# Kernel tuning notes

Hardware: AMD Instinct MI355X
Metric: run time of the kernel (lower is better)

Reference implementation:

```python
import jax, jax.numpy as jnp
import numpy as np
from jax import lax

NUM_ROUTING = 3
EPS_SQUASH = 1e-12
EPS_COS = 1e-8


def _squash(x, axis=2):
    norm = jnp.linalg.norm(x, axis=axis, keepdims=True)
    norm_sq = norm * norm
    return x / (norm + EPS_SQUASH) * (norm_sq / (1.0 + norm_sq))


def setup_inputs() -> dict:
    key = jax.random.key(0)
    k1, k2, k3 = jax.random.split(key, 3)
    B, in_dim, in_atoms, D, H, W = 2, 8, 16, 32, 32, 32
    out_dim, out_atoms, ksz = 8, 16, 3
    x = jax.random.normal(k1, (B, in_dim, in_atoms, D, H, W), dtype=jnp.float32)
    conv_w = jax.random.normal(k2, (out_dim * out_atoms, in_atoms, ksz, ksz, ksz), dtype=jnp.float32) * 0.1
    conv_b = jax.random.normal(k3, (out_dim * out_atoms,), dtype=jnp.float32) * 0.01
    biases = jnp.full((out_dim, out_atoms, 1, 1, 1), 0.1, dtype=jnp.float32)
    return {"input_tensor": x, "conv_w": conv_w, "conv_b": conv_b, "biases": biases}


def reference(input_tensor, conv_w, conv_b, biases):
    B, in_dim, in_atoms, D, H, W = input_tensor.shape
    out_dim, out_atoms = biases.shape[0], biases.shape[1]
    # DepthwiseConv4d (share_weight=True): fold (B, in_dim) into batch
    xr = input_tensor.reshape(B * in_dim, in_atoms, D, H, W)
    conv = lax.conv_general_dilated(
        xr, conv_w, window_strides=(1, 1, 1), padding=[(1, 1)] * 3,
        dimension_numbers=("NCDHW", "OIDHW", "NCDHW"))
    conv = conv + conv_b[None, :, None, None, None]
    oD, oH, oW = conv.shape[-3:]
    votes = conv.reshape(B, in_dim, out_dim, out_atoms, oD, oH, oW)
    # dynamic routing
    logits = jnp.zeros((B, in_dim, out_dim, 1, oD, oH, oW), dtype=votes.dtype)
    activation = None
    for i in range(NUM_ROUTING):
        route = jax.nn.softmax(logits, axis=2)
        # sum over input capsules (axis=1) -> [B, out_dim, out_atoms, D, H, W]
        preactivate = jnp.sum(votes * route, axis=1) + biases[None]
        if i + 1 < NUM_ROUTING:
            # cosine similarity along atoms (axis=3)
            p = preactivate[:, None]  # [B,1,out_dim,atoms,D,H,W]
            dot = jnp.sum(p * votes, axis=3)
            pn = jnp.linalg.norm(p, axis=3)
            vn = jnp.linalg.norm(votes, axis=3)
            distances = dot / jnp.maximum(pn * vn, EPS_COS)
            logits = logits + distances[:, :, :, None]
        else:
            activation = _squash(preactivate, axis=2)
    return activation
```

## Files before the change

kernel.cpp:

```cpp
#include <hip/hip_runtime.h>
#include <math.h>


typedef _Float16 half8 __attribute__((ext_vector_type(8)));
typedef _Float16 half4 __attribute__((ext_vector_type(4)));
typedef float f32x4 __attribute__((ext_vector_type(4)));
typedef float f32x2 __attribute__((ext_vector_type(2)));

__device__ __forceinline__ void gload_lds16(const void* g, void* l) {
    __builtin_amdgcn_global_load_lds(
        (const __attribute__((address_space(1))) void*)g,
        (__attribute__((address_space(3))) void*)l, 16, 0, 0);
}

__device__ __forceinline__ float swap1(float x) {
    return __builtin_bit_cast(float, __builtin_amdgcn_update_dpp(
        0, __builtin_bit_cast(int, x), 0xB1, 0xF, 0xF, true));
}
__device__ __forceinline__ f32x2 swap2(f32x2 v) {
    f32x2 r; r[0] = swap1(v[0]); r[1] = swap1(v[1]); return r;
}

__global__ __launch_bounds__(256) void prep_all(const float* __restrict__ x,
                                                const float* __restrict__ cw,
                                                _Float16* __restrict__ xt,
                                                _Float16* __restrict__ wh2) {
    __shared__ _Float16 lds[272 * 136];
    const int t   = threadIdx.x;
    const int bid = blockIdx.x;

    if (bid < 256) {
        const int b  = bid >> 7;
        const int z  = (bid >> 2) & 31;
        const int y0 = (bid & 3) << 3;
        {
            const int rw = t >> 4, u = t & 15;
            const int y = rw >> 1, wp = (rw & 1) * 33;
            *(half8*)&lds[(y * 34 + wp) * 136 + u * 8] = (half8)(_Float16)0.f;
        }
        const float* xb = x + (size_t)b * 4194304 + z * 1024 + y0 * 32;
        #pragma unroll 4
        for (int i = 0; i < 32; i++) {
            const int idx4 = i * 256 + t;
            const int ch = idx4 >> 6;
            const int y  = (idx4 >> 3) & 7;
            const int w4 = idx4 & 7;
            const f32x4 v = *(const f32x4*)(xb + (size_t)ch * 32768 + y * 32 + w4 * 4);
            const int rbase = y * 34 + w4 * 4 + 1;
            #pragma unroll
            for (int e = 0; e < 4; e++)
                lds[(rbase + e) * 136 + ch] = (_Float16)v[e];
        }
        __syncthreads();
        _Float16* dst = xt + ((size_t)((b * 34 + z + 1) * 34 + y0 + 1)) * 34 * 128;
        #pragma unroll
        for (int k = 0; k < 17; k++) {
            const int idx = k * 256 + t;
            const int vox = idx >> 4, u = idx & 15;
            *(half8*)(dst + (size_t)vox * 128 + u * 8) =
                *(const half8*)&lds[vox * 136 + u * 8];
        }
        return;
    }
    if (bid < 520) {
        const int rid = bid - 256;
        const int b = rid / 132, rr = rid - b * 132;
        int zp, yp;
        if (rr < 68) { zp = (rr >= 34) ? 33 : 0; yp = rr % 34; }
        else { const int r2 = rr - 68; zp = 1 + (r2 >> 1); yp = (r2 & 1) ? 33 : 0; }
        _Float16* dst = xt + ((size_t)((b * 34 + zp) * 34 + yp)) * 34 * 128;
        const half8 z8 = (half8)(_Float16)0.f;
        for (int idx = t; idx < 544; idx += 256)
            *(half8*)(dst + idx * 8) = z8;
        return;
    }
    {
        const int idx = (bid - 520) * 256 + t;
        const int n   = idx / 448;
        const int rem = idx - n * 448;
        const int c   = rem >> 5;
        const int k   = rem & 31;
        const int tp  = k >> 4, ca = k & 15;
        const int tap = 2 * c + tp;
        float v = (tap < 27) ? cw[n * 432 + ca * 27 + tap] : 0.0f;
        wh2[c * 4096 + n * 32 + k] = (_Float16)v;
    }
}

__global__ __launch_bounds__(512, 4) void caps_mfma_kernel(
    const _Float16* __restrict__ xt,
    const _Float16* __restrict__ wh2,
    const float* __restrict__ cb,
    const float* __restrict__ bias,
    float* __restrict__ out)
{
    __shared__ half8 slabv[4928];
    char* smem = (char*)slabv;
    _Float16* Vh = (_Float16*)slabv;
    float* RT = (float*)slabv;
    float* LG = (float*)slabv + 2304;

    const int t  = threadIdx.x;
    const int bx = blockIdx.x;
    const int gid = ((bx & 7) << 8) | (bx >> 3);
    const int h = gid & 31;
    const int d = (gid >> 5) & 31;
    const int b = gid >> 10;

    const int wid = t >> 6, lane = t & 63;

    {
        const int lrow = lane >> 4;
        const int s    = lane & 15;
        const int bzd  = b * 34 + d;
        for (int i = wid; i < 77; i += 8) {
            const int rr0 = i << 2;
            const int rr  = rr0 + lrow;
            int zy = rr / 34;
            int j  = rr - zy * 34;
            if (rr >= 306) { zy = 0; j = 0; }
            const int dz  = (zy * 11) >> 5;
            const int dy  = zy - dz * 3;
            const int uu  = s ^ (j & 15);
            const unsigned off =
                ((((unsigned)(bzd + dz) * 34u + (unsigned)(h + dy)) * 34u
                  + (unsigned)j) << 8) + (unsigned)(uu << 4);
            gload_lds16((const char*)xt + off, smem + (rr0 << 8));
        }
    }
    __syncthreads();

    const int q = lane >> 4, r = lane & 15;
    const int qlow = q & 1, tphase = q >> 1;
    const int idp = wid >> 1, chh = wid & 1;

    int zyA[14], dxA[14];
    #pragma unroll
    for (int c = 0; c < 14; c++) {
        int tap = 2 * c + tphase;
        if (tap > 26) tap = 0;
        const int dz = tap / 9, r9 = tap - dz * 9;
        const int dy = r9 / 3,  dxx = r9 - dy * 3;
        zyA[c] = dz * 3 + dy;
        dxA[c] = dxx;
    }
    const int uA0 = 4 * idp + qlow;
    const int uA1 = uA0 + 2;
    const _Float16* bp = wh2 + (chh * 64 + r) * 32 + q * 8;

    f32x4 acc[2][2][4];
    #pragma unroll
    for (int i = 0; i < 2; i++)
        #pragma unroll
        for (int j = 0; j < 2; j++)
            #pragma unroll
            for (int k = 0; k < 4; k++) acc[i][j][k] = (f32x4)0.f;

    #pragma unroll
    for (int c = 0; c < 14; c++) {
        half8 bf[4];
        #pragma unroll
        for (int nt = 0; nt < 4; nt++)
            bf[nt] = *(const half8*)(bp + c * 4096 + nt * 512);
        const int jw = r + dxA[c];
        const int js = jw & 15;
        const char* abase = smem + zyA[c] * 8704 + jw * 256;
        const char* a0 = abase + ((uA0 ^ js) << 4);
        const char* a1 = abase + ((uA1 ^ js) << 4);
        half8 af[2][2];
        af[0][0] = *(const half8*)a0;
        af[0][1] = *(const half8*)(a0 + 4096);
        af[1][0] = *(const half8*)a1;
        af[1][1] = *(const half8*)(a1 + 4096);
        #pragma unroll
        for (int jj = 0; jj < 2; jj++)
            #pragma unroll
            for (int vt = 0; vt < 2; vt++)
                #pragma unroll
                for (int nt = 0; nt < 4; nt++)
                    acc[jj][vt][nt] = __builtin_amdgcn_mfma_f32_16x16x32_f16(
                        bf[nt], af[jj][vt], acc[jj][vt][nt], 0, 0, 0);
    }

    __syncthreads();

    f32x4 cbq[4];
    #pragma unroll
    for (int nt = 0; nt < 4; nt++)
        cbq[nt] = *(const f32x4*)&cb[chh * 64 + nt * 16 + q * 4];
    #pragma unroll
    for (int jj = 0; jj < 2; jj++) {
        #pragma unroll
        for (int vt = 0; vt < 2; vt++) {
            _Float16* vp = &Vh[(vt * 16 + r) * 1032 + (2 * idp + jj) * 128
                               + chh * 64 + q * 4];
            #pragma unroll
            for (int nt = 0; nt < 4; nt++) {
                half4 hv;
                #pragma unroll
                for (int e = 0; e < 4; e++)
                    hv[e] = (_Float16)(acc[jj][vt][nt][e] + cbq[nt][e]);
                *(half4*)(vp + nt * 16) = hv;
            }
        }
    }
    __syncthreads();

    const int p = t >> 1, half = t & 1;
    const int vv = p & 31, oo = p >> 5;
    const int ib = half << 2;
    f32x2 vf2[4][8];
    #pragma unroll
    for (int ii = 0; ii < 4; ii++) {
        #pragma unroll
        for (int ah = 0; ah < 2; ah++) {
            const half8 hv =
                *(const half8*)&Vh[vv * 1032 + (ib + ii) * 128 + oo * 16 + ah * 8];
            #pragma unroll
            for (int k = 0; k < 4; k++) {
                f32x2 e; e[0] = (float)hv[2 * k]; e[1] = (float)hv[2 * k + 1];
                vf2[ii][ah * 4 + k] = e;
            }
        }
    }
    __syncthreads();

    float vn[4];
    #pragma unroll
    for (int ii = 0; ii < 4; ii++) {
        f32x2 s = (f32x2)0.f;
        #pragma unroll
        for (int k = 0; k < 8; k++)
            s = __builtin_elementwise_fma(vf2[ii][k], vf2[ii][k], s);
        vn[ii] = sqrtf(s[0] + s[1]);
    }
    f32x2 bl2[8];
    #pragma unroll
    for (int k = 0; k < 8; k++)
        bl2[k] = *(const f32x2*)&bias[oo * 16 + 2 * k];
    float rt[4], lgr[4];
    #pragma unroll
    for (int ii = 0; ii < 4; ii++) { rt[ii] = 0.125f; lgr[ii] = 0.f; }
    f32x2 pre2[8];
    for (int it = 0; it < 3; it++) {
        #pragma unroll
        for (int k = 0; k < 8; k++) pre2[k] = (f32x2)0.f;
        #pragma unroll
        for (int ii = 0; ii < 4; ii++) {
            f32x2 rtv; rtv[0] = rt[ii]; rtv[1] = rt[ii];
            #pragma unroll
            for (int k = 0; k < 8; k++)
                pre2[k] = __builtin_elementwise_fma(rtv, vf2[ii][k], pre2[k]);
        }
        #pragma unroll
        for (int k = 0; k < 8; k++)
            pre2[k] = bl2[k] + pre2[k] + swap2(pre2[k]);
        if (it == 2) break;
        f32x2 s2v = (f32x2)0.f;
        #pragma unroll
        for (int k = 0; k < 8; k++)
            s2v = __builtin_elementwise_fma(pre2[k], pre2[k], s2v);
        const float pn = sqrtf(s2v[0] + s2v[1]);
        #pragma unroll
        for (int ii = 0; ii < 4; ii++) {
            f32x2 dv = (f32x2)0.f;
            #pragma unroll
            for (int k = 0; k < 8; k++)
                dv = __builtin_elementwise_fma(pre2[k], vf2[ii][k], dv);
            lgr[ii] += __fdividef(dv[0] + dv[1], fmaxf(pn * vn[ii], 1e-8f));
            LG[vv * 72 + (ib + ii) * 8 + oo] = lgr[ii];
        }
        __syncthreads();
        {
            const f32x4 E = *(const f32x4*)&LG[vv * 72 + oo * 8 + half * 4];
            f32x4 exv; float ps = 0.f;
            #pragma unroll
            for (int k = 0; k < 4; k++) { exv[k] = __expf(E[k]); ps += exv[k]; }
            const float sum = ps + swap1(ps);
            const float rs = __fdividef(1.f, sum);
            f32x4 w4;
            #pragma unroll
            for (int k = 0; k < 4; k++) w4[k] = exv[k] * rs;
            *(f32x4*)&RT[vv * 72 + oo * 8 + half * 4] = w4;
        }
        __syncthreads();
        #pragma unroll
        for (int ii = 0; ii < 4; ii++)
            rt[ii] = RT[vv * 72 + (ib + ii) * 8 + oo];
    }
    f32x2 s2v = (f32x2)0.f;
    #pragma unroll
    for (int k = 0; k < 8; k++)
        s2v = __builtin_elementwise_fma(pre2[k], pre2[k], s2v);
    const float n2 = s2v[0] + s2v[1];
    const float nn = sqrtf(n2);
    const float scale = __fdividef(n2, (1.f + n2) * (nn + 1e-12f));
    const size_t sp = (size_t)d * 1024 + h * 32 + vv;
    #pragma unroll
    for (int a = 0; a < 8; a++) {
        const float vlo = pre2[(a >> 1)][a & 1];
        const float vhi = pre2[4 + (a >> 1)][a & 1];
        const float pv  = half ? vhi : vlo;
        out[((size_t)((b * 8 + oo) * 16 + half * 8 + a)) * 32768 + sp] = pv * scale;
    }
}

extern "C" void kernel_launch(void* const* d_in, const int* in_sizes, int n_in,
                              void* d_out, int out_size, void* d_ws, size_t ws_size,
                              hipStream_t stream) {
    const float* x    = (const float*)d_in[0];
    const float* cw   = (const float*)d_in[1];
    const float* cb   = (const float*)d_in[2];
    const float* bias = (const float*)d_in[3];
    float* out = (float*)d_out;
    _Float16* wh2 = (_Float16*)d_ws;
    _Float16* xt  = (_Float16*)((char*)d_ws + 114688);

    hipLaunchKernelGGL(prep_all, dim3(744), dim3(256), 0, stream, x, cw, xt, wh2);
    hipLaunchKernelGGL(caps_mfma_kernel, dim3(2048), dim3(512), 0, stream,
                       xt, wh2, cb, bias, out);
}
```

Baseline: 182.7 us.

## Remap routing threads to do softmax via DPP and stage output through LDS

```diff
diff --git a/kernel.cpp b/kernel.cpp
--- a/kernel.cpp
+++ b/kernel.cpp
@@ -13,13 +13,18 @@
         (__attribute__((address_space(3))) void*)l, 16, 0, 0);
 }
 
-__device__ __forceinline__ float swap1(float x) {
+template <int CTRL>
+__device__ __forceinline__ float dppf(float x) {
     return __builtin_bit_cast(float, __builtin_amdgcn_update_dpp(
-        0, __builtin_bit_cast(int, x), 0xB1, 0xF, 0xF, true));
-}
-__device__ __forceinline__ f32x2 swap2(f32x2 v) {
-    f32x2 r; r[0] = swap1(v[0]); r[1] = swap1(v[1]); return r;
-}
+        0, __builtin_bit_cast(int, x), CTRL, 0xF, 0xF, true));
+}
+__device__ __forceinline__ float sum8(float x) {
+    x += dppf<0xB1>(x);
+    x += dppf<0x4E>(x);
+    x += dppf<0x141>(x);
+    return x;
+}
+__device__ __forceinline__ float ror8f(float x) { return dppf<0x128>(x); }
 
 __global__ __launch_bounds__(256) void prep_all(const float* __restrict__ x,
                                                 const float* __restrict__ cw,
@@ -97,8 +102,7 @@
     __shared__ half8 slabv[4928];
     char* smem = (char*)slabv;
     _Float16* Vh = (_Float16*)slabv;
-    float* RT = (float*)slabv;
-    float* LG = (float*)slabv + 2304;
+    float* OF = (float*)slabv;
 
     const int t  = threadIdx.x;
     const int bx = blockIdx.x;
@@ -172,6 +176,7 @@
         af[0][1] = *(const half8*)(a0 + 4096);
         af[1][0] = *(const half8*)a1;
         af[1][1] = *(const half8*)(a1 + 4096);
+        __builtin_amdgcn_s_setprio(1);
         #pragma unroll
         for (int jj = 0; jj < 2; jj++)
             #pragma unroll
@@ -180,6 +185,7 @@
                 for (int nt = 0; nt < 4; nt++)
                     acc[jj][vt][nt] = __builtin_amdgcn_mfma_f32_16x16x32_f16(
                         bf[nt], af[jj][vt], acc[jj][vt][nt], 0, 0, 0);
+        __builtin_amdgcn_s_setprio(0);
     }
 
     __syncthreads();
@@ -206,9 +212,11 @@
     }
     __syncthreads();
 
-    const int p = t >> 1, half = t & 1;
-    const int vv = p & 31, oo = p >> 5;
-    const int ib = half << 2;
+    const int oo   = t & 7;
+    const int half = (t >> 3) & 1;
+    const int vv   = t >> 4;
+    const int ib   = half << 2;
+
     f32x2 vf2[4][8];
     #pragma unroll
     for (int ii = 0; ii < 4; ii++) {
@@ -238,10 +246,12 @@
     #pragma unroll
     for (int k = 0; k < 8; k++)
         bl2[k] = *(const f32x2*)&bias[oo * 16 + 2 * k];
+
     float rt[4], lgr[4];
     #pragma unroll
     for (int ii = 0; ii < 4; ii++) { rt[ii] = 0.125f; lgr[ii] = 0.f; }
     f32x2 pre2[8];
+
     for (int it = 0; it < 3; it++) {
         #pragma unroll
         for (int k = 0; k < 8; k++) pre2[k] = (f32x2)0.f;
@@ -253,14 +263,20 @@
                 pre2[k] = __builtin_elementwise_fma(rtv, vf2[ii][k], pre2[k]);
         }
         #pragma unroll
-        for (int k = 0; k < 8; k++)
-            pre2[k] = bl2[k] + pre2[k] + swap2(pre2[k]);
+        for (int k = 0; k < 8; k++) {
+            f32x2 cmb;
+            cmb[0] = pre2[k][0] + ror8f(pre2[k][0]);
+            cmb[1] = pre2[k][1] + ror8f(pre2[k][1]);
+            pre2[k] = bl2[k] + cmb;
+        }
         if (it == 2) break;
+
         f32x2 s2v = (f32x2)0.f;
         #pragma unroll
         for (int k = 0; k < 8; k++)
             s2v = __builtin_elementwise_fma(pre2[k], pre2[k], s2v);
         const float pn = sqrtf(s2v[0] + s2v[1]);
+
         #pragma unroll
         for (int ii = 0; ii < 4; ii++) {
             f32x2 dv = (f32x2)0.f;
@@ -268,26 +284,11 @@
             for (int k = 0; k < 8; k++)
                 dv = __builtin_elementwise_fma(pre2[k], vf2[ii][k], dv);
             lgr[ii] += __fdividef(dv[0] + dv[1], fmaxf(pn * vn[ii], 1e-8f));
-            LG[vv * 72 + (ib + ii) * 8 + oo] = lgr[ii];
-        }
-        __syncthreads();
-        {
-            const f32x4 E = *(const f32x4*)&LG[vv * 72 + oo * 8 + half * 4];
-            f32x4 exv; float ps = 0.f;
-            #pragma unroll
-            for (int k = 0; k < 4; k++) { exv[k] = __expf(E[k]); ps += exv[k]; }
-            const float sum = ps + swap1(ps);
-            const float rs = __fdividef(1.f, sum);
-            f32x4 w4;
-            #pragma unroll
-            for (int k = 0; k < 4; k++) w4[k] = exv[k] * rs;
-            *(f32x4*)&RT[vv * 72 + oo * 8 + half * 4] = w4;
-        }
-        __syncthreads();
-        #pragma unroll
-        for (int ii = 0; ii < 4; ii++)
-            rt[ii] = RT[vv * 72 + (ib + ii) * 8 + oo];
-    }
+            const float ex = __expf(lgr[ii]);
+            rt[ii] = __fdividef(ex, sum8(ex));
+        }
+    }
+
     f32x2 s2v = (f32x2)0.f;
     #pragma unroll
     for (int k = 0; k < 8; k++)
@@ -295,13 +296,24 @@
     const float n2 = s2v[0] + s2v[1];
     const float nn = sqrtf(n2);
     const float scale = __fdividef(n2, (1.f + n2) * (nn + 1e-12f));
-    const size_t sp = (size_t)d * 1024 + h * 32 + vv;
     #pragma unroll
     for (int a = 0; a < 8; a++) {
-        const float vlo = pre2[(a >> 1)][a & 1];
-        const float vhi = pre2[4 + (a >> 1)][a & 1];
-        const float pv  = half ? vhi : vlo;
-        out[((size_t)((b * 8 + oo) * 16 + half * 8 + a)) * 32768 + sp] = pv * scale;
+        const float pv = half ? pre2[4 + (a >> 1)][a & 1]
+                              : pre2[(a >> 1)][a & 1];
+        OF[vv * 130 + oo * 16 + half * 8 + a] = pv * scale;
+    }
+    __syncthreads();
+
+    #pragma unroll
+    for (int rep = 0; rep < 2; rep++) {
+        const int idx = rep * 512 + t;
+        const int ch = idx >> 3, sg = idx & 7;
+        f32x4 o0;
+        #pragma unroll
+        for (int e = 0; e < 4; e++) o0[e] = OF[(sg * 4 + e) * 130 + ch];
+        float* op = out + ((size_t)((b * 8 + (ch >> 4)) * 16 + (ch & 15))) * 32768
+                        + d * 1024 + h * 32 + sg * 4;
+        *(f32x4*)op = o0;
     }
 }
 
```

Result: faster. 174.2 us (-4.7%).
